# Performance work log

Hardware: AMD Instinct MI355X
Metric: run time of the kernel (lower is better)

The kernel has to match this reference:

```python
import jax, jax.numpy as jnp
import numpy as np

N = 20000
E = 320000
IN_DIM = 256
HID = 128
OUT = 64
HEADS = [4, 1]
NEG_SLOPE = 0.2


def setup_inputs() -> dict:
    key = jax.random.key(0)
    ks = jax.random.split(key, 12)
    x = jax.random.normal(ks[0], (N, IN_DIM), dtype=jnp.float32)
    src = jax.random.randint(ks[1], (E,), 0, N, dtype=jnp.int32)
    dst = jax.random.randint(ks[2], (E,), 0, N, dtype=jnp.int32)
    # Layer 0: in=256 -> heads=4, feat=128
    H0, D0 = HEADS[0], HID
    W1 = jax.random.normal(ks[3], (IN_DIM, H0 * D0), dtype=jnp.float32) * (1.0 / np.sqrt(IN_DIM))
    al1 = jax.random.normal(ks[4], (H0, D0), dtype=jnp.float32) * 0.1
    ar1 = jax.random.normal(ks[5], (H0, D0), dtype=jnp.float32) * 0.1
    b1 = jnp.zeros((H0 * D0,), dtype=jnp.float32)
    # Layer 1: in=4*128=512 -> heads=1, feat=64
    IN2 = H0 * D0
    H1, D1 = HEADS[1], OUT
    W2 = jax.random.normal(ks[6], (IN2, H1 * D1), dtype=jnp.float32) * (1.0 / np.sqrt(IN2))
    al2 = jax.random.normal(ks[7], (H1, D1), dtype=jnp.float32) * 0.1
    ar2 = jax.random.normal(ks[8], (H1, D1), dtype=jnp.float32) * 0.1
    b2 = jnp.zeros((H1 * D1,), dtype=jnp.float32)
    return {"x": x, "src": src, "dst": dst, "W1": W1, "al1": al1, "ar1": ar1, "b1": b1,
            "W2": W2, "al2": al2, "ar2": ar2, "b2": b2}


def gat_conv(h, src, dst, W, al, ar, b, num_heads, out_feats):
    # h: [N, F_in]; DGL GATConv, eval mode (no dropout), allow_zero_in_degree.
    feat = (h @ W).reshape(-1, num_heads, out_feats)          # [N,H,D]
    el = jnp.sum(feat * al, axis=-1)                          # [N,H]
    er = jnp.sum(feat * ar, axis=-1)                          # [N,H]
    e = jax.nn.leaky_relu(el[src] + er[dst], NEG_SLOPE)       # [E,H]
    # edge softmax over incoming edges of each dst node (numerically stable)
    m = jax.ops.segment_max(e, dst, num_segments=N)           # [N,H] (-inf for 0-in-degree)
    ex = jnp.exp(e - m[dst])                                  # [E,H]
    s = jax.ops.segment_sum(ex, dst, num_segments=N)          # [N,H]
    alpha = ex / s[dst]                                       # [E,H]
    msg = feat[src] * alpha[:, :, None]                       # [E,H,D]
    rst = jax.ops.segment_sum(msg, dst, num_segments=N)       # [N,H,D]
    return rst + b.reshape(1, num_heads, out_feats)


def reference(x, src, dst, W1, al1, ar1, b1, W2, al2, ar2, b2):
    h = gat_conv(x, src, dst, W1, al1, ar1, b1, HEADS[0], HID)   # [N,4,128]
    h = jax.nn.elu(h)                                            # activation on non-last layer
    h = h.reshape(N, HEADS[0] * HID)                             # flatten(1)
    h = gat_conv(h, src, dst, W2, al2, ar2, b2, HEADS[1], OUT)   # [N,1,64]
    return h.mean(axis=1)                                        # [N,64]
```

## Files before the change

kernel.cpp:

```cpp
#include <hip/hip_runtime.h>
#include <hip/hip_bf16.h>
#include <cstdint>
#include <cstddef>

#define N_NODES 20000
#define N_EDGES 320000
#define IN_DIM  256
#define HID     128
#define OUT_DIM 64
#define H0      4
#define CAP     64

static __device__ __forceinline__ float leaky(float x) { return x > 0.f ? x : 0.2f * x; }

using short8  = __attribute__((ext_vector_type(8))) short;
using short4v = __attribute__((ext_vector_type(4))) short;
using f32x4   = __attribute__((ext_vector_type(4))) float;

struct HL { short h; short l; };
static __device__ __forceinline__ HL split_bf16(float x) {
  HL r;
  __hip_bfloat16 hb = __float2bfloat16(x);
  float hf = __bfloat162float(hb);
  __hip_bfloat16 lb = __float2bfloat16(x - hf);
  r.h = *(short*)&hb;
  r.l = *(short*)&lb;
  return r;
}

static __device__ __forceinline__ short f2bf_bits(float x) {
  __hip_bfloat16 hb = __float2bfloat16(x);
  return *(short*)&hb;
}

static __device__ __forceinline__ float bf16bits_to_f32(short b) {
  uint32_t u = ((uint32_t)(uint16_t)b) << 16;
  return __uint_as_float(u);
}

static __device__ __forceinline__ void fma8(float a, short8 f, float* acc) {
  const uint32_t* d = (const uint32_t*)&f;
#pragma unroll
  for (int q = 0; q < 4; q++) {
    uint32_t u = d[q];
    float lo = __uint_as_float(u << 16);
    float hi = __uint_as_float(u & 0xFFFF0000u);
    acc[2 * q]     += a * lo;
    acc[2 * q + 1] += a * hi;
  }
}

__global__ void presplit_all_kernel(const float* __restrict__ x,
                                    const float* __restrict__ W1,
                                    const float* __restrict__ W2,
                                    short* __restrict__ xh,
                                    short* __restrict__ w1h, short* __restrict__ w1l,
                                    short* __restrict__ w2h, short* __restrict__ w2l,
                                    int* __restrict__ fill) {
  const int X4  = N_NODES * IN_DIM / 4;
  const int NW1 = IN_DIM * (H0 * HID);
  const int NW2 = (H0 * HID) * OUT_DIM;
  int i = blockIdx.x * 256 + threadIdx.x;
  if (i < X4) {
    int base = i * 4;
    float4 v = *(const float4*)&x[base];
    short4v hv;
    hv[0] = f2bf_bits(v.x); hv[1] = f2bf_bits(v.y);
    hv[2] = f2bf_bits(v.z); hv[3] = f2bf_bits(v.w);
    *(short4v*)&xh[base] = hv;
    return;
  }
  int j = i - X4;
  if (j < NW1) {
    int nn = j / IN_DIM, kk = j - nn * IN_DIM;
    HL e = split_bf16(W1[(size_t)kk * (H0 * HID) + nn]);
    w1h[j] = e.h; w1l[j] = e.l;
    return;
  }
  int k = j - NW1;
  if (k < NW2) {
    int nn = k / (H0 * HID), kk = k - nn * (H0 * HID);
    HL e = split_bf16(W2[(size_t)kk * OUT_DIM + nn]);
    w2h[k] = e.h; w2l[k] = e.l;
    return;
  }
  int z = k - NW2;
  if (z < N_NODES) fill[z] = 0;
}

#define LDK 40

template <int BM, int BN, int NH>
static __device__ void gemm_body(int h, int row0,
                                 const short* __restrict__ A,
                                 const short* __restrict__ Bth,
                                 const short* __restrict__ Btl,
                                 float* __restrict__ C,
                                 __hip_bfloat16* __restrict__ Cb,
                                 const float* __restrict__ alv,
                                 const float* __restrict__ arv,
                                 float* __restrict__ el,
                                 float* __restrict__ er,
                                 int M, int K) {
  constexpr int MI = BM / 32;
  constexpr int NT = BN / 32;
  constexpr int NOUT = NH * BN;
  constexpr int TPRA = 256 / BM, KPTA = 32 / TPRA;
  constexpr int TPRB = 256 / BN, KPTB = 32 / TPRB;
  __shared__ short Ash[BM * LDK];
  __shared__ short Bsh[BN * LDK];
  __shared__ short Bsl[BN * LDK];
  __shared__ float els[2][BM], ers[2][BM];
  const int tid  = threadIdx.x;
  const int lane = tid & 63;
  const int wave = tid >> 6;
  const int wm = (wave >> 1) * (BM / 2);
  const int wn = (wave & 1) * (BN / 2);
  const int lr = lane & 15;
  const int lq = lane >> 4;
  const int ra = tid / TPRA, ka = (tid % TPRA) * KPTA;
  const int rb = tid / TPRB, kb = (tid % TPRB) * KPTB;

  f32x4 acc[MI][NT];
#pragma unroll
  for (int i = 0; i < MI; i++)
#pragma unroll
    for (int j = 0; j < NT; j++) acc[i][j] = (f32x4){0.f, 0.f, 0.f, 0.f};

  for (int k0 = 0; k0 < K; k0 += 32) {
    {
      const bool ok = (row0 + ra) < M;
      const size_t g = (size_t)(row0 + ra) * K + k0 + ka;
#pragma unroll
      for (int i = 0; i < KPTA / 8; i++) {
        short8 hv = ok ? *(const short8*)&A[g + 8 * i] : (short8){0,0,0,0,0,0,0,0};
        *(short8*)&Ash[ra * LDK + ka + 8 * i] = hv;
      }
    }
    {
      const size_t g = (size_t)(h * BN + rb) * K + k0 + kb;
#pragma unroll
      for (int i = 0; i < KPTB / 8; i++) {
        short8 hv = *(const short8*)&Bth[g + 8 * i];
        short8 lv = *(const short8*)&Btl[g + 8 * i];
        *(short8*)&Bsh[rb * LDK + kb + 8 * i] = hv;
        *(short8*)&Bsl[rb * LDK + kb + 8 * i] = lv;
      }
    }
    __syncthreads();
    short8 a_v[MI], b_h[NT], b_l[NT];
#pragma unroll
    for (int mi = 0; mi < MI; mi++) {
      int r = wm + mi * 16 + lr;
      a_v[mi] = *(const short8*)&Ash[r * LDK + lq * 8];
    }
#pragma unroll
    for (int nj = 0; nj < NT; nj++) {
      int c = wn + nj * 16 + lr;
      b_h[nj] = *(const short8*)&Bsh[c * LDK + lq * 8];
      b_l[nj] = *(const short8*)&Bsl[c * LDK + lq * 8];
    }
#pragma unroll
    for (int mi = 0; mi < MI; mi++) {
#pragma unroll
      for (int nj = 0; nj < NT; nj++) {
        acc[mi][nj] = __builtin_amdgcn_mfma_f32_16x16x32_bf16(a_v[mi], b_l[nj], acc[mi][nj], 0, 0, 0);
        acc[mi][nj] = __builtin_amdgcn_mfma_f32_16x16x32_bf16(a_v[mi], b_h[nj], acc[mi][nj], 0, 0, 0);
      }
    }
    __syncthreads();
  }
  float av[NT], rv[NT];
#pragma unroll
  for (int nj = 0; nj < NT; nj++) {
    int c = h * BN + wn + nj * 16 + lr;
    av[nj] = alv[c];
    rv[nj] = arv[c];
  }
#pragma unroll
  for (int mi = 0; mi < MI; mi++) {
    float pel[4], per[4];
#pragma unroll
    for (int r = 0; r < 4; r++) {
      float se = 0.f, sr2 = 0.f;
#pragma unroll
      for (int nj = 0; nj < NT; nj++) {
        float v = acc[mi][nj][r];
        se  += v * av[nj];
        sr2 += v * rv[nj];
      }
      pel[r] = se; per[r] = sr2;
    }
#pragma unroll
    for (int off = 1; off < 16; off <<= 1) {
#pragma unroll
      for (int r = 0; r < 4; r++) {
        pel[r] += __shfl_xor(pel[r], off);
        per[r] += __shfl_xor(per[r], off);
      }
    }
    int rowb = wm + mi * 16 + lq * 4;
    if (lr == 0) {
#pragma unroll
      for (int r = 0; r < 4; r++) {
        els[wave & 1][rowb + r] = pel[r];
        ers[wave & 1][rowb + r] = per[r];
      }
    }
    int row = row0 + rowb;
#pragma unroll
    for (int r = 0; r < 4; r++) {
      if (row + r < M) {
#pragma unroll
        for (int nj = 0; nj < NT; nj++) {
          float val = acc[mi][nj][r];
          size_t idx = (size_t)(row + r) * NOUT + h * BN + wn + nj * 16 + lr;
          if (C)  C[idx] = val;
          if (Cb) Cb[idx] = __float2bfloat16(val);
        }
      }
    }
  }
  __syncthreads();
  if (tid < BM && row0 + tid < M) {
    el[(size_t)(row0 + tid) * NH + h] = els[0][tid] + els[1][tid];
    er[(size_t)(row0 + tid) * NH + h] = ers[0][tid] + ers[1][tid];
  }
}

#define GEMM0_BLOCKS (H0 * ((N_NODES + 127) / 128))
#define FILL_BLOCKS  ((N_EDGES + 255) / 256)

__global__ __launch_bounds__(256) void fill_gemm0_kernel(
    const int* __restrict__ src, const int* __restrict__ dst,
    int* __restrict__ fill, int* __restrict__ csr_src,
    const short* __restrict__ xh,
    const short* __restrict__ w1h, const short* __restrict__ w1l,
    __hip_bfloat16* __restrict__ feat1b,
    const float* __restrict__ al1, const float* __restrict__ ar1,
    float* __restrict__ el1, float* __restrict__ er1) {
  if (blockIdx.x < GEMM0_BLOCKS) {
    int h = blockIdx.x & 3;
    int row0 = (blockIdx.x >> 2) * 128;
    gemm_body<128, 128, 4>(h, row0, xh, w1h, w1l, (float*)nullptr, feat1b,
                           al1, ar1, el1, er1, N_NODES, IN_DIM);
    return;
  }
  int e = (blockIdx.x - GEMM0_BLOCKS) * 256 + threadIdx.x;
  if (e < N_EDGES) {
    int d = dst[e];
    int p = atomicAdd(&fill[d], 1);
    if (p < CAP) csr_src[d * CAP + p] = src[e];
  }
}

__global__ __launch_bounds__(256) void gemm1_kernel(
    const short* __restrict__ h1b,
    const short* __restrict__ w2h, const short* __restrict__ w2l,
    float* __restrict__ feat2,
    const float* __restrict__ al2, const float* __restrict__ ar2,
    float* __restrict__ el2, float* __restrict__ er2) {
  gemm_body<64, 64, 1>(0, blockIdx.x * 64, h1b, w2h, w2l, feat2,
                       (__hip_bfloat16*)nullptr, al2, ar2, el2, er2,
                       N_NODES, H0 * HID);
}

__global__ __launch_bounds__(256) void coef0_kernel(const int* __restrict__ fillc,
                                                    const int* __restrict__ csr_src,
                                                    const float* __restrict__ el,
                                                    const float* __restrict__ er,
                                                    float* __restrict__ alphaT) {
  int w = threadIdx.x >> 6;
  int n = blockIdx.x * 4 + w;
  int lane = threadIdx.x & 63;
  if (n >= N_NODES) return;
  int deg = min(fillc[n], CAP);
  int start = n * CAP;
  float4 er4 = *(const float4*)&er[n * 4];

  float4 ev = make_float4(-1e30f, -1e30f, -1e30f, -1e30f);
  int sv = 0;
  if (lane < deg) {
    sv = csr_src[start + lane];
    float4 l4 = *(const float4*)&el[sv * 4];
    ev.x = leaky(l4.x + er4.x); ev.y = leaky(l4.y + er4.y);
    ev.z = leaky(l4.z + er4.z); ev.w = leaky(l4.w + er4.w);
  }
  float4 m = ev;
#pragma unroll
  for (int off = 32; off; off >>= 1) {
    m.x = fmaxf(m.x, __shfl_xor(m.x, off));
    m.y = fmaxf(m.y, __shfl_xor(m.y, off));
    m.z = fmaxf(m.z, __shfl_xor(m.z, off));
    m.w = fmaxf(m.w, __shfl_xor(m.w, off));
  }
  float4 ex = make_float4(0.f, 0.f, 0.f, 0.f);
  if (lane < deg) {
    ex.x = __expf(ev.x - m.x); ex.y = __expf(ev.y - m.y);
    ex.z = __expf(ev.z - m.z); ex.w = __expf(ev.w - m.w);
  }
  float4 ss = ex;
#pragma unroll
  for (int off = 32; off; off >>= 1) {
    ss.x += __shfl_xor(ss.x, off);
    ss.y += __shfl_xor(ss.y, off);
    ss.z += __shfl_xor(ss.z, off);
    ss.w += __shfl_xor(ss.w, off);
  }
  if (lane < deg) {
    const int NC = N_NODES * CAP;
    int p = start + lane;
    alphaT[0 * NC + p] = ex.x / ss.x;
    alphaT[1 * NC + p] = ex.y / ss.y;
    alphaT[2 * NC + p] = ex.z / ss.z;
    alphaT[3 * NC + p] = ex.w / ss.w;
  }
}

__global__ __launch_bounds__(256) void agg0s_kernel(const int* __restrict__ fillc,
                                                    const int* __restrict__ csr_src,
                                                    const float* __restrict__ alphaT,
                                                    const __hip_bfloat16* __restrict__ featb,
                                                    const float* __restrict__ bias,
                                                    short* __restrict__ h1b) {
  int s  = blockIdx.x & 7;
  int nb = blockIdx.x >> 3;
  int tid = threadIdx.x;
  int j = tid >> 3;
  int q = tid & 7;
  int n = nb * 32 + j;
  int h = s >> 1;

  __shared__ int2 as_s[32][CAP];

  int deg = 0;
  if (n < N_NODES) deg = min(fillc[n], CAP);
  int start = n * CAP;
  const int NC = N_NODES * CAP;
  for (int slot = q; slot < deg; slot += 8) {
    int2 v;
    v.x = csr_src[start + slot];
    v.y = __float_as_int(alphaT[h * NC + start + slot]);
    as_s[j][slot] = v;
  }
  __syncthreads();

  const short* fb = (const short*)featb;
  const int fofs = s * 64 + q * 8;
  float acc[8] = {};
  for (int i = 0; i < deg; i++) {
    int2 v = as_s[j][i];
    short8 f = *(const short8*)&fb[(v.x << 9) + fofs];
    fma8(__int_as_float(v.y), f, acc);
  }

  if (n < N_NODES) {
    short8 ob;
#pragma unroll
    for (int jj = 0; jj < 8; jj++) {
      float o = acc[jj] + bias[fofs + jj];
      o = o > 0.f ? o : (__expf(o) - 1.f);
      ob[jj] = f2bf_bits(o);
    }
    *(short8*)&h1b[((size_t)n << 9) + fofs] = ob;
  }
}

__global__ __launch_bounds__(256) void agg1_kernel(const int* __restrict__ fillc,
                                                   const int* __restrict__ csr_src,
                                                   const float* __restrict__ el,
                                                   const float* __restrict__ er,
                                                   const float* __restrict__ feat,
                                                   const float* __restrict__ bias,
                                                   float* __restrict__ out) {
  __shared__ float alpha_s[4][64];
  __shared__ int   src_s[4][64];
  int w = threadIdx.x >> 6;
  int n = blockIdx.x * 4 + w;
  int lane = threadIdx.x & 63;
  if (n >= N_NODES) return;
  int deg = min(fillc[n], CAP);
  int start = n * CAP;
  float erd = er[n];
  int g = lane >> 4, q = lane & 15;
  float4 acc = make_float4(0.f, 0.f, 0.f, 0.f);

  float ev = -1e30f; int sv = 0;
  if (lane < deg) { sv = csr_src[start + lane]; ev = leaky(el[sv] + erd); }
  float m = ev;
#pragma unroll
  for (int off = 32; off; off >>= 1) m = fmaxf(m, __shfl_xor(m, off));
  float ex = (lane < deg) ? __expf(ev - m) : 0.f;
  float ss = ex;
#pragma unroll
  for (int off = 32; off; off >>= 1) ss += __shfl_xor(ss, off);
  if (lane < deg) { alpha_s[w][lane] = ex / ss; src_s[w][lane] = sv; }

  if (deg > 0) {
    int nit = (deg + 3) >> 2;
    float a_c = 0.f;
    float4 f_c = make_float4(0.f, 0.f, 0.f, 0.f);
    {
      int e = g;
      if (e < deg) {
        a_c = alpha_s[w][e];
        int s = src_s[w][e];
        f_c = *(const float4*)&feat[(size_t)s * OUT_DIM + q * 4];
      }
    }
    for (int it = 1; it < nit; it++) {
      float a_n = 0.f;
      float4 f_n = make_float4(0.f, 0.f, 0.f, 0.f);
      int e = (it << 2) + g;
      if (e < deg) {
        a_n = alpha_s[w][e];
        int s = src_s[w][e];
        f_n = *(const float4*)&feat[(size_t)s * OUT_DIM + q * 4];
      }
      acc.x += a_c * f_c.x; acc.y += a_c * f_c.y;
      acc.z += a_c * f_c.z; acc.w += a_c * f_c.w;
      a_c = a_n; f_c = f_n;
    }
    acc.x += a_c * f_c.x; acc.y += a_c * f_c.y;
    acc.z += a_c * f_c.z; acc.w += a_c * f_c.w;
  }

#pragma unroll
  for (int off = 16; off < 64; off <<= 1) {
    acc.x += __shfl_xor(acc.x, off);
    acc.y += __shfl_xor(acc.y, off);
    acc.z += __shfl_xor(acc.z, off);
    acc.w += __shfl_xor(acc.w, off);
  }
  if (g == 0) {
    float4 b4 = *(const float4*)&bias[q * 4];
    float4 o = make_float4(acc.x + b4.x, acc.y + b4.y, acc.z + b4.z, acc.w + b4.w);
    *(float4*)&out[(size_t)n * OUT_DIM + q * 4] = o;
  }
}

extern "C" void kernel_launch(void* const* d_in, const int* in_sizes, int n_in,
                              void* d_out, int out_size, void* d_ws, size_t ws_size,
                              hipStream_t stream) {
  const float* x   = (const float*)d_in[0];
  const int*   src = (const int*)d_in[1];
  const int*   dst = (const int*)d_in[2];
  const float* W1  = (const float*)d_in[3];
  const float* al1 = (const float*)d_in[4];
  const float* ar1 = (const float*)d_in[5];
  const float* b1  = (const float*)d_in[6];
  const float* W2  = (const float*)d_in[7];
  const float* al2 = (const float*)d_in[8];
  const float* ar2 = (const float*)d_in[9];
  const float* b2  = (const float*)d_in[10];

  char* ws = (char*)d_ws;
  size_t off = 0;
  auto alloc = [&](size_t bytes) -> void* {
    void* p = ws + off;
    off += (bytes + 255) & ~(size_t)255;
    return p;
  };
  int* fill     = (int*)alloc((size_t)N_NODES * 4);
  int* csr_src  = (int*)alloc((size_t)N_NODES * CAP * 4);
  short* xh     = (short*)alloc((size_t)N_NODES * IN_DIM * 2);
  short* W1th   = (short*)alloc((size_t)IN_DIM * (H0 * HID) * 2);
  short* W1tl   = (short*)alloc((size_t)IN_DIM * (H0 * HID) * 2);
  short* W2th   = (short*)alloc((size_t)(H0 * HID) * OUT_DIM * 2);
  short* W2tl   = (short*)alloc((size_t)(H0 * HID) * OUT_DIM * 2);
  __hip_bfloat16* feat1b = (__hip_bfloat16*)alloc((size_t)N_NODES * (H0 * HID) * 2);
  float* el1    = (float*)alloc((size_t)N_NODES * H0 * 4);
  float* er1    = (float*)alloc((size_t)N_NODES * H0 * 4);
  float* alphaT = (float*)alloc((size_t)H0 * N_NODES * CAP * 4);
  short* h1b    = (short*)alloc((size_t)N_NODES * (H0 * HID) * 2);
  float* feat2  = (float*)alloc((size_t)N_NODES * OUT_DIM * 4);
  float* el2    = (float*)alloc((size_t)N_NODES * 4);
  float* er2    = (float*)alloc((size_t)N_NODES * 4);
  (void)ws_size; (void)in_sizes; (void)n_in; (void)out_size;

  {
    const int total = N_NODES * IN_DIM / 4 + IN_DIM * (H0 * HID) + (H0 * HID) * OUT_DIM
                    + N_NODES;
    presplit_all_kernel<<<(total + 255) / 256, 256, 0, stream>>>(
        x, W1, W2, xh, W1th, W1tl, W2th, W2tl, fill);
  }

  fill_gemm0_kernel<<<GEMM0_BLOCKS + FILL_BLOCKS, 256, 0, stream>>>(
      src, dst, fill, csr_src, xh, W1th, W1tl, feat1b, al1, ar1, el1, er1);

  coef0_kernel<<<(N_NODES + 3) / 4, 256, 0, stream>>>(fill, csr_src, el1, er1, alphaT);

  agg0s_kernel<<<((N_NODES + 31) / 32) * 8, 256, 0, stream>>>(
      fill, csr_src, alphaT, feat1b, b1, h1b);

  gemm1_kernel<<<(N_NODES + 63) / 64, 256, 0, stream>>>(h1b, W2th, W2tl, feat2, al2, ar2, el2, er2);

  agg1_kernel<<<(N_NODES + 3) / 4, 256, 0, stream>>>(fill, csr_src, el2, er2, feat2, b2, (float*)d_out);
}
```

Baseline: 185.7 us.

## Fuse layer-0 edge softmax into aggregation kernel and prefetch neighbor features

Removes the separate coefficient kernel and its alphaT buffer. Each aggregation thread group now computes the per-head max and sum of exponentials over its node's incoming edges with 8-lane shuffles. It stores unnormalized exponentials in shared memory and applies the 1/sum factor once at output. The gather loop also loads the next neighbor's feature vector before doing the current FMA. In exchange, attention logits are recomputed by each of the two blocks covering a head, and the block barrier is dropped in favour of relying on intra-wave ordering of shared-memory writes and reads.

```diff
diff --git a/kernel.cpp b/kernel.cpp
--- a/kernel.cpp
+++ b/kernel.cpp
@@ -265,61 +265,10 @@
                        N_NODES, H0 * HID);
 }
 
-__global__ __launch_bounds__(256) void coef0_kernel(const int* __restrict__ fillc,
+__global__ __launch_bounds__(256) void agg0s_kernel(const int* __restrict__ fillc,
                                                     const int* __restrict__ csr_src,
                                                     const float* __restrict__ el,
                                                     const float* __restrict__ er,
-                                                    float* __restrict__ alphaT) {
-  int w = threadIdx.x >> 6;
-  int n = blockIdx.x * 4 + w;
-  int lane = threadIdx.x & 63;
-  if (n >= N_NODES) return;
-  int deg = min(fillc[n], CAP);
-  int start = n * CAP;
-  float4 er4 = *(const float4*)&er[n * 4];
-
-  float4 ev = make_float4(-1e30f, -1e30f, -1e30f, -1e30f);
-  int sv = 0;
-  if (lane < deg) {
-    sv = csr_src[start + lane];
-    float4 l4 = *(const float4*)&el[sv * 4];
-    ev.x = leaky(l4.x + er4.x); ev.y = leaky(l4.y + er4.y);
-    ev.z = leaky(l4.z + er4.z); ev.w = leaky(l4.w + er4.w);
-  }
-  float4 m = ev;
-#pragma unroll
-  for (int off = 32; off; off >>= 1) {
-    m.x = fmaxf(m.x, __shfl_xor(m.x, off));
-    m.y = fmaxf(m.y, __shfl_xor(m.y, off));
-    m.z = fmaxf(m.z, __shfl_xor(m.z, off));
-    m.w = fmaxf(m.w, __shfl_xor(m.w, off));
-  }
-  float4 ex = make_float4(0.f, 0.f, 0.f, 0.f);
-  if (lane < deg) {
-    ex.x = __expf(ev.x - m.x); ex.y = __expf(ev.y - m.y);
-    ex.z = __expf(ev.z - m.z); ex.w = __expf(ev.w - m.w);
-  }
-  float4 ss = ex;
-#pragma unroll
-  for (int off = 32; off; off >>= 1) {
-    ss.x += __shfl_xor(ss.x, off);
-    ss.y += __shfl_xor(ss.y, off);
-    ss.z += __shfl_xor(ss.z, off);
-    ss.w += __shfl_xor(ss.w, off);
-  }
-  if (lane < deg) {
-    const int NC = N_NODES * CAP;
-    int p = start + lane;
-    alphaT[0 * NC + p] = ex.x / ss.x;
-    alphaT[1 * NC + p] = ex.y / ss.y;
-    alphaT[2 * NC + p] = ex.z / ss.z;
-    alphaT[3 * NC + p] = ex.w / ss.w;
-  }
-}
-
-__global__ __launch_bounds__(256) void agg0s_kernel(const int* __restrict__ fillc,
-                                                    const int* __restrict__ csr_src,
-                                                    const float* __restrict__ alphaT,
                                                     const __hip_bfloat16* __restrict__ featb,
                                                     const float* __restrict__ bias,
                                                     short* __restrict__ h1b) {
@@ -333,32 +282,52 @@
 
   __shared__ int2 as_s[32][CAP];
 
-  int deg = 0;
-  if (n < N_NODES) deg = min(fillc[n], CAP);
+  bool valid = (n < N_NODES);
+  int deg = valid ? min(fillc[n], CAP) : 0;
   int start = n * CAP;
-  const int NC = N_NODES * CAP;
+
+  float erd = valid ? er[n * 4 + h] : 0.f;
+  float mx = -1e30f;
   for (int slot = q; slot < deg; slot += 8) {
-    int2 v;
-    v.x = csr_src[start + slot];
-    v.y = __float_as_int(alphaT[h * NC + start + slot]);
+    int sv = csr_src[start + slot];
+    mx = fmaxf(mx, leaky(el[sv * 4 + h] + erd));
+  }
+  mx = fmaxf(mx, __shfl_xor(mx, 1));
+  mx = fmaxf(mx, __shfl_xor(mx, 2));
+  mx = fmaxf(mx, __shfl_xor(mx, 4));
+  float ss = 0.f;
+  for (int slot = q; slot < deg; slot += 8) {
+    int sv = csr_src[start + slot];
+    float ex = __expf(leaky(el[sv * 4 + h] + erd) - mx);
+    ss += ex;
+    int2 v; v.x = sv; v.y = __float_as_int(ex);
     as_s[j][slot] = v;
   }
-  __syncthreads();
+  ss += __shfl_xor(ss, 1);
+  ss += __shfl_xor(ss, 2);
+  ss += __shfl_xor(ss, 4);
+  float inv = (deg > 0) ? (1.0f / ss) : 0.f;
 
   const short* fb = (const short*)featb;
   const int fofs = s * 64 + q * 8;
   float acc[8] = {};
-  for (int i = 0; i < deg; i++) {
-    int2 v = as_s[j][i];
-    short8 f = *(const short8*)&fb[(v.x << 9) + fofs];
-    fma8(__int_as_float(v.y), f, acc);
-  }
-
-  if (n < N_NODES) {
+  if (deg > 0) {
+    int2 v0 = as_s[j][0];
+    short8 f0 = *(const short8*)&fb[(v0.x << 9) + fofs];
+    for (int i = 1; i < deg; i++) {
+      int2 v1 = as_s[j][i];
+      short8 f1 = *(const short8*)&fb[(v1.x << 9) + fofs];
+      fma8(__int_as_float(v0.y), f0, acc);
+      v0 = v1; f0 = f1;
+    }
+    fma8(__int_as_float(v0.y), f0, acc);
+  }
+
+  if (valid) {
     short8 ob;
 #pragma unroll
     for (int jj = 0; jj < 8; jj++) {
-      float o = acc[jj] + bias[fofs + jj];
+      float o = acc[jj] * inv + bias[fofs + jj];
       o = o > 0.f ? o : (__expf(o) - 1.f);
       ob[jj] = f2bf_bits(o);
     }
@@ -471,7 +440,6 @@
   __hip_bfloat16* feat1b = (__hip_bfloat16*)alloc((size_t)N_NODES * (H0 * HID) * 2);
   float* el1    = (float*)alloc((size_t)N_NODES * H0 * 4);
   float* er1    = (float*)alloc((size_t)N_NODES * H0 * 4);
-  float* alphaT = (float*)alloc((size_t)H0 * N_NODES * CAP * 4);
   short* h1b    = (short*)alloc((size_t)N_NODES * (H0 * HID) * 2);
   float* feat2  = (float*)alloc((size_t)N_NODES * OUT_DIM * 4);
   float* el2    = (float*)alloc((size_t)N_NODES * 4);
@@ -488,10 +456,8 @@
   fill_gemm0_kernel<<<GEMM0_BLOCKS + FILL_BLOCKS, 256, 0, stream>>>(
       src, dst, fill, csr_src, xh, W1th, W1tl, feat1b, al1, ar1, el1, er1);
 
-  coef0_kernel<<<(N_NODES + 3) / 4, 256, 0, stream>>>(fill, csr_src, el1, er1, alphaT);
-
   agg0s_kernel<<<((N_NODES + 31) / 32) * 8, 256, 0, stream>>>(
-      fill, csr_src, alphaT, feat1b, b1, h1b);
+      fill, csr_src, el1, er1, feat1b, b1, h1b);
 
   gemm1_kernel<<<(N_NODES + 63) / 64, 256, 0, stream>>>(h1b, W2th, W2tl, feat2, al2, ar2, el2, er2);
 
```

New measurement: 187.6 us. Within noise of the previous version (+1.0%).
